# Kernel tuning notes

Hardware: AMD Instinct MI355X
Metric: run time of the kernel (lower is better)

Reference implementation:

```python
import jax, jax.numpy as jnp
import numpy as np

B, C, N, K = 16, 128, 1024, 16
QK_DIM, V_DIM = 64, 128


def setup_inputs() -> dict:
    key = jax.random.key(0)
    k1, k2, k3, k4, k5 = jax.random.split(key, 5)
    return {
        "input_tensor": jax.random.normal(k1, (B, C, N, K), dtype=jnp.float32),
        "W_qk": jax.random.normal(k2, (2 * QK_DIM, C), dtype=jnp.float32) * 0.05,
        "b_qk": jax.random.normal(k3, (2 * QK_DIM,), dtype=jnp.float32) * 0.01,
        "W_v": jax.random.normal(k4, (V_DIM, C), dtype=jnp.float32) * 0.05,
        "b_v": jax.random.normal(k5, (V_DIM,), dtype=jnp.float32) * 0.01,
        "qk_dim": QK_DIM,
    }


def reference(input_tensor, W_qk, b_qk, W_v, b_v, qk_dim):
    # 1x1 conv == channel matmul: [B,C,N,K] x [2*qk,C] -> [B,2*qk,N,K]
    combine = jnp.einsum('bcnk,oc->bonk', input_tensor, W_qk) + b_qk[None, :, None, None]
    q = combine[:, :qk_dim]          # [B, qk, N, K]
    k = combine[:, qk_dim:]          # [B, qk, N, K]
    # per-point attention over neighbor axis
    energy = jnp.einsum('bcnq,bcnk->bnqk', q, k)            # [B, N, K, K]
    scale = jnp.asarray(qk_dim, energy.dtype) ** 0.5
    attention = jax.nn.softmax(energy / scale, axis=3)       # softmax over last k
    v = jnp.einsum('bcnk,oc->bonk', input_tensor, W_v) + b_v[None, :, None, None]  # [B, v, N, K]
    attention_first = attention[:, :, :, 0]                  # [B, N, K] (q-axis slice at k=0)
    # out = einsum('bnk,bcnk->bnkc') then sum over k -> fuse into one einsum
    output = jnp.einsum('bnk,bcnk->bnc', attention_first, v) # [B, N, v_dim]
    return output
```

## Files before the change

kernel.cpp:

```cpp
#include <hip/hip_runtime.h>
#include <hip/hip_bf16.h>
#include <stdint.h>

typedef __attribute__((ext_vector_type(4))) float f32x4;
typedef __attribute__((ext_vector_type(8))) short s16x8;

__device__ __forceinline__ unsigned int pack_bf2(float lo, float hi) {
  union { __hip_bfloat162 h; unsigned int u; } cv;
  cv.h = __float22bfloat162_rn(float2{lo, hi});
  return cv.u;
}
__device__ __forceinline__ float bflo(unsigned int w) { return __uint_as_float(w << 16); }
__device__ __forceinline__ float bfhi(unsigned int w) { return __uint_as_float(w & 0xFFFF0000u); }

union FragU { uint4 u; s16x8 s; };

__global__ void __launch_bounds__(256) prep_weights(const float* __restrict__ Wqk,
                                                    const float* __restrict__ Wv,
                                                    uint16_t* __restrict__ wsqk,
                                                    uint16_t* __restrict__ wsv) {
  int i = blockIdx.x * 256 + threadIdx.x;
  if (i < 16384) {
    union { __hip_bfloat16 h; uint16_t u; } c; c.h = __float2bfloat16(Wqk[i]);
    wsqk[i] = c.u;
  } else if (i < 32768) {
    int j = i - 16384;
    union { __hip_bfloat16 h; uint16_t u; } c; c.h = __float2bfloat16(Wv[j]);
    wsv[j] = c.u;
  }
}

__global__ void __launch_bounds__(256, 4) attn_kernel(
    const float* __restrict__ X,
    const float* __restrict__ bqk,
    const float* __restrict__ bv,
    const unsigned int* __restrict__ wqk,
    const unsigned int* __restrict__ wv,
    float* __restrict__ out)
{
  __shared__ unsigned int sXt[64 * 68];
  __shared__ unsigned int sP[64 * 68];
  __shared__ float sa[4][16];
  __shared__ float sS[4];

  const int t    = threadIdx.x;
  const int lane = t & 63;
  const int w    = t >> 6;
  const int nn   = lane & 15;
  const int quad = lane >> 4;

  const int b  = blockIdx.x >> 8;
  const int n0 = (blockIdx.x & 255) << 2;

  {
    const int j4 = t & 15;
    const int cb = t >> 4;
    #pragma unroll
    for (int it = 0; it < 8; ++it) {
      const int c = cb + it * 16;
      const float4 v = *reinterpret_cast<const float4*>(
          X + ((size_t)(b * 128 + c) * 1024 + n0) * 16 + j4 * 4);
      uint2 pk;
      pk.x = pack_bf2(v.x, v.y);
      pk.y = pack_bf2(v.z, v.w);
      *reinterpret_cast<uint2*>(&sP[c * 32 + j4 * 2]) = pk;
    }
  }
  __syncthreads();

  {
    const int jp = t & 31;
    const int cg = t >> 5;
    #pragma unroll
    for (int s = 0; s < 2; ++s) {
      const int ch = (cg + 8 * s + jp) & 15;
      unsigned int wd[8];
      #pragma unroll
      for (int i = 0; i < 8; ++i) wd[i] = sP[(ch * 8 + i) * 32 + jp];
      uint4 lo, hi;
      lo.x = (wd[0] & 0xFFFFu) | (wd[1] << 16);
      lo.y = (wd[2] & 0xFFFFu) | (wd[3] << 16);
      lo.z = (wd[4] & 0xFFFFu) | (wd[5] << 16);
      lo.w = (wd[6] & 0xFFFFu) | (wd[7] << 16);
      hi.x = (wd[0] >> 16) | (wd[1] & 0xFFFF0000u);
      hi.y = (wd[2] >> 16) | (wd[3] & 0xFFFF0000u);
      hi.z = (wd[4] >> 16) | (wd[5] & 0xFFFF0000u);
      hi.w = (wd[6] >> 16) | (wd[7] & 0xFFFF0000u);
      *reinterpret_cast<uint4*>(&sXt[(2 * jp) * 68 + ch * 4]) = lo;
      *reinterpret_cast<uint4*>(&sXt[(2 * jp + 1) * 68 + ch * 4]) = hi;
    }
  }
  __syncthreads();

  f32x4 acc[8];
  {
    #pragma unroll
    for (int mt = 0; mt < 8; ++mt) {
      const float4 bq = *reinterpret_cast<const float4*>(bqk + mt * 16 + quad * 4);
      acc[mt][0] = bq.x; acc[mt][1] = bq.y; acc[mt][2] = bq.z; acc[mt][3] = bq.w;
    }
    #pragma unroll
    for (int ks = 0; ks < 4; ++ks) {
      FragU bfr;
      bfr.u = *reinterpret_cast<const uint4*>(&sXt[(w * 16 + nn) * 68 + ks * 16 + quad * 4]);
      #pragma unroll
      for (int mt = 0; mt < 8; ++mt) {
        FragU af;
        af.u = *reinterpret_cast<const uint4*>(wqk + (mt * 16 + nn) * 64 + ks * 16 + quad * 4);
        acc[mt] = __builtin_amdgcn_mfma_f32_16x16x32_bf16(af.s, bfr.s, acc[mt], 0, 0, 0);
      }
    }
  }

  {
    #pragma unroll
    for (int mt = 0; mt < 8; ++mt) {
      uint2 pr;
      pr.x = pack_bf2(acc[mt][0], acc[mt][1]);
      pr.y = pack_bf2(acc[mt][2], acc[mt][3]);
      *reinterpret_cast<uint2*>(&sP[(w * 16 + nn) * 68 + mt * 8 + quad * 2]) = pr;
    }
  }

  float aq[16];
  float Ssum;
  {
    f32x4 e = {0.f, 0.f, 0.f, 0.f};
    #pragma unroll
    for (int ks = 0; ks < 2; ++ks) {
      FragU qa, kb;
      qa.u = *reinterpret_cast<const uint4*>(&sP[(w * 16 + nn) * 68 + ks * 16 + quad * 4]);
      kb.u = *reinterpret_cast<const uint4*>(&sP[(w * 16 + nn) * 68 + 32 + ks * 16 + quad * 4]);
      e = __builtin_amdgcn_mfma_f32_16x16x32_bf16(qa.s, kb.s, e, 0, 0, 0);
    }
    #pragma unroll
    for (int r = 0; r < 4; ++r) {
      float l = e[r] * 0.125f;
      float mx = l;
      mx = fmaxf(mx, __shfl_xor(mx, 1));
      mx = fmaxf(mx, __shfl_xor(mx, 2));
      mx = fmaxf(mx, __shfl_xor(mx, 4));
      mx = fmaxf(mx, __shfl_xor(mx, 8));
      float pe = __expf(l - mx);
      float ss = pe;
      ss += __shfl_xor(ss, 1);
      ss += __shfl_xor(ss, 2);
      ss += __shfl_xor(ss, 4);
      ss += __shfl_xor(ss, 8);
      if (nn == 0) sa[w][quad * 4 + r] = pe / ss;
    }
    Ssum = 0.f;
    #pragma unroll
    for (int k = 0; k < 16; ++k) { aq[k] = sa[w][k]; Ssum += aq[k]; }
  }

  unsigned int* sYw = &sP[w * 16 * 68];
  {
    float y0 = 0.f, y1 = 0.f;
    #pragma unroll
    for (int k = 0; k < 16; ++k) {
      const unsigned int xw = sXt[(w * 16 + k) * 68 + lane];
      y0 += aq[k] * bflo(xw);
      y1 += aq[k] * bfhi(xw);
    }
    sYw[lane] = pack_bf2(y0, y1);
    if (lane == 0) sS[w] = Ssum;
  }
  __syncthreads();

  {
    #pragma unroll
    for (int i = 0; i < 2; ++i) {
      const int ct = w * 2 + i;
      f32x4 z = {0.f, 0.f, 0.f, 0.f};
      #pragma unroll
      for (int ks = 0; ks < 4; ++ks) {
        FragU av2, by;
        av2.u = *reinterpret_cast<const uint4*>(wv + (ct * 16 + nn) * 64 + ks * 16 + quad * 4);
        by.u  = *reinterpret_cast<const uint4*>(&sP[(nn & 3) * 16 * 68 + ks * 16 + quad * 4]);
        z = __builtin_amdgcn_mfma_f32_16x16x32_bf16(av2.s, by.s, z, 0, 0, 0);
      }
      if (nn < 4) {
        const float4 bvv = *reinterpret_cast<const float4*>(bv + ct * 16 + quad * 4);
        const float S = sS[nn];
        float4 o4;
        o4.x = z[0] + bvv.x * S;
        o4.y = z[1] + bvv.y * S;
        o4.z = z[2] + bvv.z * S;
        o4.w = z[3] + bvv.w * S;
        *reinterpret_cast<float4*>(out + (size_t)(b * 1024 + n0 + nn) * 128 + ct * 16 + quad * 4) = o4;
      }
    }
  }
}

extern "C" void kernel_launch(void* const* d_in, const int* in_sizes, int n_in,
                              void* d_out, int out_size, void* d_ws, size_t ws_size,
                              hipStream_t stream) {
  (void)in_sizes; (void)n_in; (void)out_size; (void)ws_size;
  const float* X   = (const float*)d_in[0];
  const float* Wqk = (const float*)d_in[1];
  const float* bqk = (const float*)d_in[2];
  const float* Wv  = (const float*)d_in[3];
  const float* bv  = (const float*)d_in[4];

  uint16_t* wsqk = (uint16_t*)d_ws;
  uint16_t* wsv  = wsqk + 16384;

  prep_weights<<<128, 256, 0, stream>>>(Wqk, Wv, wsqk, wsv);
  attn_kernel<<<4096, 256, 0, stream>>>(X, bqk, bv,
                                        (const unsigned int*)wsqk,
                                        (const unsigned int*)wsv,
                                        (float*)d_out);
}
```

Before: 254.6 us.

## Load X directly into MFMA fragments, dropping LDS staging transpose and barriers

Each wave now reads its own point's input as per-lane scalar loads laid out as the MFMA B-operand fragment, converting to bf16 in registers. It still writes the fragment to LDS for the later value-weighting step. This removes the block-wide float4 staging pass, the LDS bit-shuffle transpose and two __syncthreads, so the QK matmul can start as soon as the wave's loads arrive. The trade-off is four times as many global load instructions (dword instead of dwordx4), each touching only 64-byte contiguous segments per channel, which may reduce memory efficiency.

```diff
diff --git a/kernel.cpp b/kernel.cpp
--- a/kernel.cpp
+++ b/kernel.cpp
@@ -51,46 +51,25 @@
 
   const int b  = blockIdx.x >> 8;
   const int n0 = (blockIdx.x & 255) << 2;
+  const int n  = n0 + w;
 
+  FragU xf[4];
   {
-    const int j4 = t & 15;
-    const int cb = t >> 4;
+    const float* __restrict__ xb = X + (size_t)b * (128 * 1024 * 16) + n * 16 + nn;
     #pragma unroll
-    for (int it = 0; it < 8; ++it) {
-      const int c = cb + it * 16;
-      const float4 v = *reinterpret_cast<const float4*>(
-          X + ((size_t)(b * 128 + c) * 1024 + n0) * 16 + j4 * 4);
-      uint2 pk;
-      pk.x = pack_bf2(v.x, v.y);
-      pk.y = pack_bf2(v.z, v.w);
-      *reinterpret_cast<uint2*>(&sP[c * 32 + j4 * 2]) = pk;
+    for (int ks = 0; ks < 4; ++ks) {
+      const int c0 = ks * 32 + quad * 8;
+      float v[8];
+      #pragma unroll
+      for (int i = 0; i < 8; ++i)
+        v[i] = xb[(size_t)(c0 + i) * (1024 * 16)];
+      xf[ks].u.x = pack_bf2(v[0], v[1]);
+      xf[ks].u.y = pack_bf2(v[2], v[3]);
+      xf[ks].u.z = pack_bf2(v[4], v[5]);
+      xf[ks].u.w = pack_bf2(v[6], v[7]);
+      *reinterpret_cast<uint4*>(&sXt[(w * 16 + nn) * 68 + ks * 16 + quad * 4]) = xf[ks].u;
     }
   }
-  __syncthreads();
-
-  {
-    const int jp = t & 31;
-    const int cg = t >> 5;
-    #pragma unroll
-    for (int s = 0; s < 2; ++s) {
-      const int ch = (cg + 8 * s + jp) & 15;
-      unsigned int wd[8];
-      #pragma unroll
-      for (int i = 0; i < 8; ++i) wd[i] = sP[(ch * 8 + i) * 32 + jp];
-      uint4 lo, hi;
-      lo.x = (wd[0] & 0xFFFFu) | (wd[1] << 16);
-      lo.y = (wd[2] & 0xFFFFu) | (wd[3] << 16);
-      lo.z = (wd[4] & 0xFFFFu) | (wd[5] << 16);
-      lo.w = (wd[6] & 0xFFFFu) | (wd[7] << 16);
-      hi.x = (wd[0] >> 16) | (wd[1] & 0xFFFF0000u);
-      hi.y = (wd[2] >> 16) | (wd[3] & 0xFFFF0000u);
-      hi.z = (wd[4] >> 16) | (wd[5] & 0xFFFF0000u);
-      hi.w = (wd[6] >> 16) | (wd[7] & 0xFFFF0000u);
-      *reinterpret_cast<uint4*>(&sXt[(2 * jp) * 68 + ch * 4]) = lo;
-      *reinterpret_cast<uint4*>(&sXt[(2 * jp + 1) * 68 + ch * 4]) = hi;
-    }
-  }
-  __syncthreads();
 
   f32x4 acc[8];
   {
@@ -101,13 +80,11 @@
     }
     #pragma unroll
     for (int ks = 0; ks < 4; ++ks) {
-      FragU bfr;
-      bfr.u = *reinterpret_cast<const uint4*>(&sXt[(w * 16 + nn) * 68 + ks * 16 + quad * 4]);
       #pragma unroll
       for (int mt = 0; mt < 8; ++mt) {
         FragU af;
         af.u = *reinterpret_cast<const uint4*>(wqk + (mt * 16 + nn) * 64 + ks * 16 + quad * 4);
-        acc[mt] = __builtin_amdgcn_mfma_f32_16x16x32_bf16(af.s, bfr.s, acc[mt], 0, 0, 0);
+        acc[mt] = __builtin_amdgcn_mfma_f32_16x16x32_bf16(af.s, xf[ks].s, acc[mt], 0, 0, 0);
       }
     }
   }
```

Result: no change. 253.6 us (-0.4%).
